# Kernel tuning notes

Hardware: AMD Instinct MI355X
Metric: run time of the kernel (lower is better)

The kernel has to match this reference:

```python
import jax, jax.numpy as jnp
import numpy as np

B, S, D, H = 4, 2048, 1024, 16
HD = D // H  # head_size = 64
SCALE = HD ** -0.5


def setup_inputs() -> dict:
    key = jax.random.key(0)
    k1, k2, k3 = jax.random.split(key, 3)
    hidden_states = jax.random.normal(k1, (B, S, D), dtype=jnp.float32)
    W_qkv = jax.random.normal(k2, (D, 3 * D), dtype=jnp.float32) * 0.02
    W_out = jax.random.normal(k3, (D, D), dtype=jnp.float32) * 0.02
    return {"hidden_states": hidden_states, "W_qkv": W_qkv, "W_out": W_out}


def reference(hidden_states, W_qkv, W_out):
    b, s, d = hidden_states.shape
    qkv = hidden_states @ W_qkv                      # [b, s, 3d]
    q, k, v = jnp.split(qkv, 3, axis=-1)
    # [b, s, d] -> [b, H, s, hd]
    q = q.reshape(b, s, H, HD).transpose(0, 2, 1, 3)
    k = k.reshape(b, s, H, HD).transpose(0, 2, 1, 3)
    v = v.reshape(b, s, H, HD).transpose(0, 2, 1, 3)
    scores = jnp.einsum("bhqd,bhkd->bhqk", q, k) * SCALE  # [b, H, s, s]
    probs = jax.nn.softmax(scores, axis=-1)
    ctx = jnp.einsum("bhqk,bhkd->bhqd", probs, v)         # [b, H, s, hd]
    ctx = ctx.transpose(0, 2, 1, 3).reshape(b, s, d)
    out = ctx @ W_out
    return out
```

## Files before the change

### kernel.cpp

```cpp
#include <hip/hip_runtime.h>

typedef __attribute__((ext_vector_type(8))) __bf16 bf8;
typedef __attribute__((ext_vector_type(4))) float f4;
typedef __attribute__((ext_vector_type(8))) unsigned short us8;
typedef __attribute__((ext_vector_type(4))) unsigned short us4;
typedef __attribute__((ext_vector_type(4))) unsigned int u32x4;
typedef __attribute__((ext_vector_type(2))) unsigned int u32x2;

#define MFMA16(a, b, c) __builtin_amdgcn_mfma_f32_16x16x32_bf16((a), (b), (c), 0, 0, 0)
#define GLOAD16(gp, lp)                                                        \
  __builtin_amdgcn_global_load_lds(                                            \
      (const __attribute__((address_space(1))) void*)(gp),                     \
      (__attribute__((address_space(3))) void*)(lp), 16, 0, 0)

__device__ __forceinline__ unsigned short f2bf(float f) {
  unsigned u = __builtin_bit_cast(unsigned, f);
  u += 0x7FFFu + ((u >> 16) & 1u);
  return (unsigned short)(u >> 16);
}

__device__ __forceinline__ float fexp2(float x) {
  float r;
  asm("v_exp_f32 %0, %1" : "=v"(r) : "v"(x));
  return r;
}

__device__ __forceinline__ unsigned cvtpk(float a, float b) {
  unsigned r;
  asm("v_cvt_pk_bf16_f32 %0, %1, %2" : "=v"(r) : "v"(a), "v"(b));
  return r;
}

__global__ __launch_bounds__(256) void c_cast(const float* __restrict__ in,
                                              unsigned short* __restrict__ out) {
  int i = blockIdx.x * 256 + threadIdx.x;
  const float4* p = reinterpret_cast<const float4*>(in) + (size_t)i * 2;
  float4 a = p[0], b = p[1];
  us8 o;
  o[0] = f2bf(a.x); o[1] = f2bf(a.y); o[2] = f2bf(a.z); o[3] = f2bf(a.w);
  o[4] = f2bf(b.x); o[5] = f2bf(b.y); o[6] = f2bf(b.z); o[7] = f2bf(b.w);
  *reinterpret_cast<us8*>(&out[(size_t)i * 8]) = o;
}

__global__ __launch_bounds__(256) void c_trans(const float* __restrict__ in,
                                               unsigned short* __restrict__ out,
                                               int R, int C) {
  __shared__ float T[64][65];
  const int t = threadIdx.x;
  const int c0 = blockIdx.x * 64, r0 = blockIdx.y * 64;
  const int tr = t >> 4, tc = (t & 15) * 4;
#pragma unroll
  for (int i = 0; i < 4; ++i) {
    int r = tr + i * 16;
    float4 v = *reinterpret_cast<const float4*>(&in[(size_t)(r0 + r) * C + c0 + tc]);
    T[r][tc] = v.x; T[r][tc + 1] = v.y; T[r][tc + 2] = v.z; T[r][tc + 3] = v.w;
  }
  __syncthreads();
#pragma unroll
  for (int i = 0; i < 4; ++i) {
    int c = tr + i * 16;
    us4 o;
    o[0] = f2bf(T[tc + 0][c]); o[1] = f2bf(T[tc + 1][c]);
    o[2] = f2bf(T[tc + 2][c]); o[3] = f2bf(T[tc + 3][c]);
    *reinterpret_cast<us4*>(&out[(size_t)(c0 + c) * R + r0 + tc]) = o;
  }
}

__global__ __launch_bounds__(256) void k_qkv(const unsigned short* __restrict__ A,
                                             const unsigned short* __restrict__ Bt,
                                             unsigned short* __restrict__ Qo,
                                             unsigned short* __restrict__ Ko,
                                             unsigned short* __restrict__ Vo) {
  __shared__ unsigned short As[2][128 * 32];
  __shared__ unsigned short Bs[2][128 * 32];
  const int t = threadIdx.x;
  const int lane = t & 63, wid = t >> 6;
  const int wr = wid >> 1, wc = wid & 1;
  const int cl = lane & 15, kr8 = (lane >> 4) << 3;
  const int m0 = blockIdx.x << 7, n0 = blockIdx.y << 7;

  f4 acc[4][4];
#pragma unroll
  for (int i = 0; i < 4; ++i)
#pragma unroll
    for (int j = 0; j < 4; ++j) acc[i][j] = (f4){0.f, 0.f, 0.f, 0.f};

  auto STAGE = [&](int buf, int kt) {
    int k0 = kt << 5;
#pragma unroll
    for (int it = 0; it < 2; ++it) {
      int c = t + (it << 8);
      int wb = (t & 192) + (it << 8);
      GLOAD16(A + (size_t)(m0 + (c >> 2)) * 1024 + k0 + ((c & 3) << 3),
              (char*)As[buf] + (size_t)wb * 16);
      GLOAD16(Bt + (size_t)(n0 + (c >> 2)) * 1024 + k0 + ((c & 3) << 3),
              (char*)Bs[buf] + (size_t)wb * 16);
    }
  };

  STAGE(0, 0);
  __syncthreads();
  for (int kt = 0; kt < 32; ++kt) {
    int cur = kt & 1;
    if (kt < 31) STAGE(cur ^ 1, kt + 1);
    const unsigned short* as = As[cur];
    const unsigned short* bs = Bs[cur];
    bf8 af[4], bfr[4];
#pragma unroll
    for (int mi = 0; mi < 4; ++mi)
      af[mi] = *reinterpret_cast<const bf8*>(&as[(wr * 64 + mi * 16 + cl) * 32 + kr8]);
#pragma unroll
    for (int ni = 0; ni < 4; ++ni)
      bfr[ni] = *reinterpret_cast<const bf8*>(&bs[(wc * 64 + ni * 16 + cl) * 32 + kr8]);
#pragma unroll
    for (int mi = 0; mi < 4; ++mi)
#pragma unroll
      for (int ni = 0; ni < 4; ++ni)
        acc[mi][ni] = MFMA16(af[mi], bfr[ni], acc[mi][ni]);
    __syncthreads();
  }

#pragma unroll
  for (int mi = 0; mi < 4; ++mi) {
#pragma unroll
    for (int ni = 0; ni < 4; ++ni) {
      int gcol = n0 + wc * 64 + ni * 16 + cl;
      int grow0 = m0 + wr * 64 + mi * 16 + ((lane >> 4) << 2);
      int b = grow0 >> 11, s0 = grow0 & 2047;
      if (gcol < 1024) {
        int h = gcol >> 6, hd = gcol & 63;
#pragma unroll
        for (int r = 0; r < 4; ++r)
          Qo[((size_t)(b * 16 + h) * 2048 + s0 + r) * 64 + hd] =
              f2bf(acc[mi][ni][r] * 0.18033688011112042f);
      } else if (gcol < 2048) {
        int cc = gcol - 1024;
        int h = cc >> 6, hd = cc & 63;
#pragma unroll
        for (int r = 0; r < 4; ++r)
          Ko[((size_t)(b * 16 + h) * 2048 + s0 + r) * 64 + hd] = f2bf(acc[mi][ni][r]);
      } else {
        int cc = gcol - 2048;
        int h = cc >> 6, hd = cc & 63;
        us4 o;
        o[0] = f2bf(acc[mi][ni][0]); o[1] = f2bf(acc[mi][ni][1]);
        o[2] = f2bf(acc[mi][ni][2]); o[3] = f2bf(acc[mi][ni][3]);
        *reinterpret_cast<us4*>(&Vo[((size_t)(b * 16 + h) * 64 + hd) * 2048 + s0]) = o;
      }
    }
  }
}

__global__ __launch_bounds__(512) void k_attn(const unsigned short* __restrict__ Q,
                                              const unsigned short* __restrict__ K,
                                              const unsigned short* __restrict__ Vt,
                                              unsigned short* __restrict__ Ctx) {
  __shared__ __align__(16) unsigned short Ks[2][64 * 64];
  __shared__ __align__(16) unsigned short Vs[2][64 * 64];
  const int t = threadIdx.x;
  const int lane = t & 63, wid = t >> 6;
  const int cl = lane & 15, g = lane >> 4;
  const int bh = blockIdx.y, b = bh >> 4, h = bh & 15;
  const int q0 = blockIdx.x << 7;
  const size_t base = (size_t)bh * (2048 * 64);

  const int qrow = q0 + wid * 16 + cl;
  bf8 qf0 = *reinterpret_cast<const bf8*>(&Q[base + (size_t)qrow * 64 + (g << 3)]);
  bf8 qf1 = *reinterpret_cast<const bf8*>(&Q[base + (size_t)qrow * 64 + 32 + (g << 3)]);

  const unsigned ones_u = 0x3F803F80u;
  u32x4 ones4 = (u32x4){ones_u, ones_u, ones_u, ones_u};
  bf8 onesb = __builtin_bit_cast(bf8, ones4);
  const f4 minit = (f4){-12.f, -12.f, -12.f, -12.f};

  f4 o[4], osum;
#pragma unroll
  for (int n = 0; n < 4; ++n) o[n] = (f4){0.f, 0.f, 0.f, 0.f};
  osum = (f4){0.f, 0.f, 0.f, 0.f};

  auto STAGEK = [&](int buf, int kv0) {
    int kvl = t >> 3;
    int dblk = (t & 7) ^ (kvl & 7);
    GLOAD16(K + base + (size_t)(kv0 + kvl) * 64 + (dblk << 3),
            (char*)Ks[buf] + (size_t)(t & 448) * 16);
  };
  auto STAGEV = [&](int buf, int kv0) {
    int d = t >> 3, ch = t & 7;
    int kq = ch ^ ((d >> 1) & 7);
    GLOAD16(Vt + base + (size_t)d * 2048 + kv0 + (kq << 3),
            (char*)Vs[buf] + (size_t)(t & 448) * 16);
  };

  STAGEK(0, 0);
  STAGEV(0, 0);
  __syncthreads();

  for (int tk = 0; tk < 32; ++tk) {
    int cur = tk & 1;
    if (tk < 31) {
      STAGEK(cur ^ 1, (tk + 1) << 6);
      STAGEV(cur ^ 1, (tk + 1) << 6);
    }
    const char* kp = (const char*)Ks[cur];
    const char* vp = (const char*)Vs[cur];

    f4 sT[4];
    __builtin_amdgcn_s_setprio(1);
#pragma unroll
    for (int cb = 0; cb < 4; ++cb) {
      int row = cb * 16 + cl;
      bf8 a0 = *reinterpret_cast<const bf8*>(kp + row * 128 + ((g ^ (cl & 7)) << 4));
      bf8 a1 = *reinterpret_cast<const bf8*>(kp + row * 128 + (((4 + g) ^ (cl & 7)) << 4));
      f4 s = minit;
      s = MFMA16(a0, qf0, s);
      s = MFMA16(a1, qf1, s);
      sT[cb] = s;
    }
    __builtin_amdgcn_s_setprio(0);

    u32x4 pa0, pa1;
    pa0[0] = cvtpk(fexp2(sT[0][0]), fexp2(sT[0][1]));
    pa0[1] = cvtpk(fexp2(sT[0][2]), fexp2(sT[0][3]));
    pa0[2] = cvtpk(fexp2(sT[1][0]), fexp2(sT[1][1]));
    pa0[3] = cvtpk(fexp2(sT[1][2]), fexp2(sT[1][3]));
    pa1[0] = cvtpk(fexp2(sT[2][0]), fexp2(sT[2][1]));
    pa1[1] = cvtpk(fexp2(sT[2][2]), fexp2(sT[2][3]));
    pa1[2] = cvtpk(fexp2(sT[3][0]), fexp2(sT[3][1]));
    pa1[3] = cvtpk(fexp2(sT[3][2]), fexp2(sT[3][3]));
    bf8 paA = __builtin_bit_cast(bf8, pa0);
    bf8 paB = __builtin_bit_cast(bf8, pa1);

    unsigned vb0 = (unsigned)(cl * 128) + (unsigned)((g ^ (cl & 14)) << 3);
    __builtin_amdgcn_s_setprio(1);
#pragma unroll
    for (int n = 0; n < 4; ++n) {
      unsigned a00 = vb0 + (unsigned)(n * 2048);
      u32x2 lo0 = *reinterpret_cast<const u32x2*>(vp + a00);
      u32x2 hi0 = *reinterpret_cast<const u32x2*>(vp + (a00 ^ 32u));
      u32x2 lo1 = *reinterpret_cast<const u32x2*>(vp + (a00 ^ 64u));
      u32x2 hi1 = *reinterpret_cast<const u32x2*>(vp + (a00 ^ 96u));
      u32x4 b0 = (u32x4){lo0[0], lo0[1], hi0[0], hi0[1]};
      u32x4 b1 = (u32x4){lo1[0], lo1[1], hi1[0], hi1[1]};
      o[n] = MFMA16(paA, __builtin_bit_cast(bf8, b0), o[n]);
      o[n] = MFMA16(paB, __builtin_bit_cast(bf8, b1), o[n]);
    }
    osum = MFMA16(paA, onesb, osum);
    osum = MFMA16(paB, onesb, osum);
    __builtin_amdgcn_s_setprio(0);

    __syncthreads();
  }

#pragma unroll
  for (int r = 0; r < 4; ++r) {
    float inv = 1.0f / osum[r];
    int s = q0 + wid * 16 + (g << 2) + r;
    size_t rb = ((size_t)b * 2048 + s) * 1024 + h * 64;
#pragma unroll
    for (int n = 0; n < 4; ++n) Ctx[rb + n * 16 + cl] = f2bf(o[n][r] * inv);
  }
}

__global__ __launch_bounds__(256) void k_oproj(const unsigned short* __restrict__ A,
                                               const unsigned short* __restrict__ Bt,
                                               float* __restrict__ Out) {
  __shared__ unsigned short As[2][128 * 32];
  __shared__ unsigned short Bs[2][128 * 32];
  const int t = threadIdx.x;
  const int lane = t & 63, wid = t >> 6;
  const int wr = wid >> 1, wc = wid & 1;
  const int cl = lane & 15, kr8 = (lane >> 4) << 3;
  const int m0 = blockIdx.x << 7, n0 = blockIdx.y << 7;

  f4 acc[4][4];
#pragma unroll
  for (int i = 0; i < 4; ++i)
#pragma unroll
    for (int j = 0; j < 4; ++j) acc[i][j] = (f4){0.f, 0.f, 0.f, 0.f};

  auto STAGE = [&](int buf, int kt) {
    int k0 = kt << 5;
#pragma unroll
    for (int it = 0; it < 2; ++it) {
      int c = t + (it << 8);
      int wb = (t & 192) + (it << 8);
      GLOAD16(A + (size_t)(m0 + (c >> 2)) * 1024 + k0 + ((c & 3) << 3),
              (char*)As[buf] + (size_t)wb * 16);
      GLOAD16(Bt + (size_t)(n0 + (c >> 2)) * 1024 + k0 + ((c & 3) << 3),
              (char*)Bs[buf] + (size_t)wb * 16);
    }
  };

  STAGE(0, 0);
  __syncthreads();
  for (int kt = 0; kt < 32; ++kt) {
    int cur = kt & 1;
    if (kt < 31) STAGE(cur ^ 1, kt + 1);
    const unsigned short* as = As[cur];
    const unsigned short* bs = Bs[cur];
    bf8 af[4], bfr[4];
#pragma unroll
    for (int mi = 0; mi < 4; ++mi)
      af[mi] = *reinterpret_cast<const bf8*>(&as[(wr * 64 + mi * 16 + cl) * 32 + kr8]);
#pragma unroll
    for (int ni = 0; ni < 4; ++ni)
      bfr[ni] = *reinterpret_cast<const bf8*>(&bs[(wc * 64 + ni * 16 + cl) * 32 + kr8]);
#pragma unroll
    for (int mi = 0; mi < 4; ++mi)
#pragma unroll
      for (int ni = 0; ni < 4; ++ni)
        acc[mi][ni] = MFMA16(af[mi], bfr[ni], acc[mi][ni]);
    __syncthreads();
  }

#pragma unroll
  for (int mi = 0; mi < 4; ++mi) {
#pragma unroll
    for (int ni = 0; ni < 4; ++ni) {
      int gcol = n0 + wc * 64 + ni * 16 + cl;
#pragma unroll
      for (int r = 0; r < 4; ++r) {
        int grow = m0 + wr * 64 + mi * 16 + ((lane >> 4) << 2) + r;
        Out[(size_t)grow * 1024 + gcol] = acc[mi][ni][r];
      }
    }
  }
}

extern "C" void kernel_launch(void* const* d_in, const int* in_sizes, int n_in,
                              void* d_out, int out_size, void* d_ws, size_t ws_size,
                              hipStream_t stream) {
  const float* hs = (const float*)d_in[0];
  const float* wqkv = (const float*)d_in[1];
  const float* wout = (const float*)d_in[2];
  float* out = (float*)d_out;

  unsigned short* ws = (unsigned short*)d_ws;
  const size_t NHS = (size_t)8192 * 1024;
  const size_t NWQ = (size_t)1024 * 3072;
  const size_t NWO = (size_t)1024 * 1024;
  const size_t NQ = (size_t)64 * 2048 * 64;

  unsigned short* hsb = ws;
  unsigned short* wqt = ws + NHS;
  unsigned short* wot = wqt + NWQ;
  unsigned short* Qw = wot + NWO;
  unsigned short* Kw = Qw + NQ;
  unsigned short* Vw = Kw + NQ;
  unsigned short* Cw = hsb;

  c_cast<<<dim3(4096), 256, 0, stream>>>(hs, hsb);
  c_trans<<<dim3(48, 16), 256, 0, stream>>>(wqkv, wqt, 1024, 3072);
  c_trans<<<dim3(16, 16), 256, 0, stream>>>(wout, wot, 1024, 1024);
  k_qkv<<<dim3(64, 24), 256, 0, stream>>>(hsb, wqt, Qw, Kw, Vw);
  k_attn<<<dim3(16, 64), 512, 0, stream>>>(Qw, Kw, Vw, Cw);
  k_oproj<<<dim3(64, 8), 256, 0, stream>>>(Cw, wot, out);
}
```

Before: 212.3 us.

## Split attention KV tile across wave pairs with 32 query rows per wave

Each wave now owns 32 query rows and half of each 64-key tile, so every K and V fragment read from LDS is reused across two query sub-tiles. This halves LDS fragment traffic per MFMA. The cost is doubled accumulator registers and a cross-wave reduction through shared memory at the end, where the odd waves write partial outputs and row sums for the even waves to add.

```diff
diff --git a/kernel.cpp b/kernel.cpp
--- a/kernel.cpp
+++ b/kernel.cpp
@@ -155,40 +155,48 @@
                                               const unsigned short* __restrict__ K,
                                               const unsigned short* __restrict__ Vt,
                                               unsigned short* __restrict__ Ctx) {
-  __shared__ __align__(16) unsigned short Ks[2][64 * 64];
-  __shared__ __align__(16) unsigned short Vs[2][64 * 64];
+  __shared__ __align__(16) unsigned short SMEM[2][2][64 * 64];
+  __shared__ float RedS[128];
   const int t = threadIdx.x;
   const int lane = t & 63, wid = t >> 6;
   const int cl = lane & 15, g = lane >> 4;
+  const int qg = wid >> 1, kg = wid & 1;
   const int bh = blockIdx.y, b = bh >> 4, h = bh & 15;
   const int q0 = blockIdx.x << 7;
   const size_t base = (size_t)bh * (2048 * 64);
 
-  const int qrow = q0 + wid * 16 + cl;
-  bf8 qf0 = *reinterpret_cast<const bf8*>(&Q[base + (size_t)qrow * 64 + (g << 3)]);
-  bf8 qf1 = *reinterpret_cast<const bf8*>(&Q[base + (size_t)qrow * 64 + 32 + (g << 3)]);
+  bf8 qf[2][2];
+#pragma unroll
+  for (int qi = 0; qi < 2; ++qi) {
+    int qrow = q0 + qg * 32 + qi * 16 + cl;
+    qf[qi][0] = *reinterpret_cast<const bf8*>(&Q[base + (size_t)qrow * 64 + (g << 3)]);
+    qf[qi][1] = *reinterpret_cast<const bf8*>(&Q[base + (size_t)qrow * 64 + 32 + (g << 3)]);
+  }
 
   const unsigned ones_u = 0x3F803F80u;
   u32x4 ones4 = (u32x4){ones_u, ones_u, ones_u, ones_u};
   bf8 onesb = __builtin_bit_cast(bf8, ones4);
   const f4 minit = (f4){-12.f, -12.f, -12.f, -12.f};
 
-  f4 o[4], osum;
-#pragma unroll
-  for (int n = 0; n < 4; ++n) o[n] = (f4){0.f, 0.f, 0.f, 0.f};
-  osum = (f4){0.f, 0.f, 0.f, 0.f};
+  f4 o[2][4], osum[2];
+#pragma unroll
+  for (int qi = 0; qi < 2; ++qi) {
+#pragma unroll
+    for (int n = 0; n < 4; ++n) o[qi][n] = (f4){0.f, 0.f, 0.f, 0.f};
+    osum[qi] = (f4){0.f, 0.f, 0.f, 0.f};
+  }
 
   auto STAGEK = [&](int buf, int kv0) {
     int kvl = t >> 3;
     int dblk = (t & 7) ^ (kvl & 7);
     GLOAD16(K + base + (size_t)(kv0 + kvl) * 64 + (dblk << 3),
-            (char*)Ks[buf] + (size_t)(t & 448) * 16);
+            (char*)SMEM[0][buf] + (size_t)(t & 448) * 16);
   };
   auto STAGEV = [&](int buf, int kv0) {
     int d = t >> 3, ch = t & 7;
     int kq = ch ^ ((d >> 1) & 7);
     GLOAD16(Vt + base + (size_t)d * 2048 + kv0 + (kq << 3),
-            (char*)Vs[buf] + (size_t)(t & 448) * 16);
+            (char*)SMEM[1][buf] + (size_t)(t & 448) * 16);
   };
 
   STAGEK(0, 0);
@@ -201,63 +209,93 @@
       STAGEK(cur ^ 1, (tk + 1) << 6);
       STAGEV(cur ^ 1, (tk + 1) << 6);
     }
-    const char* kp = (const char*)Ks[cur];
-    const char* vp = (const char*)Vs[cur];
-
-    f4 sT[4];
+    const char* kp = (const char*)SMEM[0][cur];
+    const char* vp = (const char*)SMEM[1][cur];
+
+    f4 sT[2][2];
     __builtin_amdgcn_s_setprio(1);
 #pragma unroll
-    for (int cb = 0; cb < 4; ++cb) {
-      int row = cb * 16 + cl;
+    for (int cb = 0; cb < 2; ++cb) {
+      int row = (2 * kg + cb) * 16 + cl;
       bf8 a0 = *reinterpret_cast<const bf8*>(kp + row * 128 + ((g ^ (cl & 7)) << 4));
       bf8 a1 = *reinterpret_cast<const bf8*>(kp + row * 128 + (((4 + g) ^ (cl & 7)) << 4));
-      f4 s = minit;
-      s = MFMA16(a0, qf0, s);
-      s = MFMA16(a1, qf1, s);
-      sT[cb] = s;
+#pragma unroll
+      for (int qi = 0; qi < 2; ++qi) {
+        f4 s = minit;
+        s = MFMA16(a0, qf[qi][0], s);
+        s = MFMA16(a1, qf[qi][1], s);
+        sT[cb][qi] = s;
+      }
     }
     __builtin_amdgcn_s_setprio(0);
 
-    u32x4 pa0, pa1;
-    pa0[0] = cvtpk(fexp2(sT[0][0]), fexp2(sT[0][1]));
-    pa0[1] = cvtpk(fexp2(sT[0][2]), fexp2(sT[0][3]));
-    pa0[2] = cvtpk(fexp2(sT[1][0]), fexp2(sT[1][1]));
-    pa0[3] = cvtpk(fexp2(sT[1][2]), fexp2(sT[1][3]));
-    pa1[0] = cvtpk(fexp2(sT[2][0]), fexp2(sT[2][1]));
-    pa1[1] = cvtpk(fexp2(sT[2][2]), fexp2(sT[2][3]));
-    pa1[2] = cvtpk(fexp2(sT[3][0]), fexp2(sT[3][1]));
-    pa1[3] = cvtpk(fexp2(sT[3][2]), fexp2(sT[3][3]));
-    bf8 paA = __builtin_bit_cast(bf8, pa0);
-    bf8 paB = __builtin_bit_cast(bf8, pa1);
-
-    unsigned vb0 = (unsigned)(cl * 128) + (unsigned)((g ^ (cl & 14)) << 3);
+    u32x4 pw[2];
+#pragma unroll
+    for (int qi = 0; qi < 2; ++qi) {
+      pw[qi][0] = cvtpk(fexp2(sT[0][qi][0]), fexp2(sT[0][qi][1]));
+      pw[qi][1] = cvtpk(fexp2(sT[0][qi][2]), fexp2(sT[0][qi][3]));
+      pw[qi][2] = cvtpk(fexp2(sT[1][qi][0]), fexp2(sT[1][qi][1]));
+      pw[qi][3] = cvtpk(fexp2(sT[1][qi][2]), fexp2(sT[1][qi][3]));
+    }
+    bf8 pa0 = __builtin_bit_cast(bf8, pw[0]);
+    bf8 pa1 = __builtin_bit_cast(bf8, pw[1]);
+
+    const int q1 = 8 * kg + g, q2 = 8 * kg + 4 + g;
+    unsigned vb = (unsigned)(cl * 128);
+    unsigned o1 = (unsigned)((q1 ^ (cl & 14)) << 3);
+    unsigned o2 = (unsigned)((q2 ^ (cl & 14)) << 3);
     __builtin_amdgcn_s_setprio(1);
 #pragma unroll
     for (int n = 0; n < 4; ++n) {
-      unsigned a00 = vb0 + (unsigned)(n * 2048);
-      u32x2 lo0 = *reinterpret_cast<const u32x2*>(vp + a00);
-      u32x2 hi0 = *reinterpret_cast<const u32x2*>(vp + (a00 ^ 32u));
-      u32x2 lo1 = *reinterpret_cast<const u32x2*>(vp + (a00 ^ 64u));
-      u32x2 hi1 = *reinterpret_cast<const u32x2*>(vp + (a00 ^ 96u));
-      u32x4 b0 = (u32x4){lo0[0], lo0[1], hi0[0], hi0[1]};
-      u32x4 b1 = (u32x4){lo1[0], lo1[1], hi1[0], hi1[1]};
-      o[n] = MFMA16(paA, __builtin_bit_cast(bf8, b0), o[n]);
-      o[n] = MFMA16(paB, __builtin_bit_cast(bf8, b1), o[n]);
-    }
-    osum = MFMA16(paA, onesb, osum);
-    osum = MFMA16(paB, onesb, osum);
+      unsigned a = vb + (unsigned)(n * 2048);
+      u32x2 lo = *reinterpret_cast<const u32x2*>(vp + a + o1);
+      u32x2 hi = *reinterpret_cast<const u32x2*>(vp + a + o2);
+      u32x4 bw = (u32x4){lo[0], lo[1], hi[0], hi[1]};
+      bf8 vb8 = __builtin_bit_cast(bf8, bw);
+      o[0][n] = MFMA16(pa0, vb8, o[0][n]);
+      o[1][n] = MFMA16(pa1, vb8, o[1][n]);
+    }
+    osum[0] = MFMA16(pa0, onesb, osum[0]);
+    osum[1] = MFMA16(pa1, onesb, osum[1]);
     __builtin_amdgcn_s_setprio(0);
 
     __syncthreads();
   }
 
-#pragma unroll
-  for (int r = 0; r < 4; ++r) {
-    float inv = 1.0f / osum[r];
-    int s = q0 + wid * 16 + (g << 2) + r;
-    size_t rb = ((size_t)b * 2048 + s) * 1024 + h * 64;
-#pragma unroll
-    for (int n = 0; n < 4; ++n) Ctx[rb + n * 16 + cl] = f2bf(o[n][r] * inv);
+  float* red = (float*)SMEM;
+  if (kg) {
+#pragma unroll
+    for (int qi = 0; qi < 2; ++qi) {
+#pragma unroll
+      for (int n = 0; n < 4; ++n) {
+        int ridx = qg * 8 + qi * 4 + n;
+        *reinterpret_cast<f4*>(red + ridx * 256 + cl * 16 + g * 4) = o[qi][n];
+      }
+      if (cl == 0)
+        *reinterpret_cast<f4*>(&RedS[(qg * 2 + qi) * 16 + g * 4]) = osum[qi];
+    }
+  }
+  __syncthreads();
+  if (!kg) {
+#pragma unroll
+    for (int qi = 0; qi < 2; ++qi) {
+#pragma unroll
+      for (int n = 0; n < 4; ++n) {
+        int ridx = qg * 8 + qi * 4 + n;
+        f4 po = *reinterpret_cast<const f4*>(red + ridx * 256 + cl * 16 + g * 4);
+        o[qi][n] += po;
+      }
+      f4 ps = *reinterpret_cast<const f4*>(&RedS[(qg * 2 + qi) * 16 + g * 4]);
+      osum[qi] += ps;
+#pragma unroll
+      for (int r = 0; r < 4; ++r) {
+        float inv = 1.0f / osum[qi][r];
+        int s = q0 + qg * 32 + qi * 16 + (g << 2) + r;
+        size_t rb = ((size_t)b * 2048 + s) * 1024 + h * 64;
+#pragma unroll
+        for (int n = 0; n < 4; ++n) Ctx[rb + n * 16 + cl] = f2bf(o[qi][n][r] * inv);
+      }
+    }
   }
 }
 
```

Result: faster. 197.4 us (-7.0%).
